# Optimization experiments

Hardware: AMD Instinct MI355X
Metric: run time of the kernel (lower is better)

The kernel has to match this reference:

```python
import jax, jax.numpy as jnp
import numpy as np


def _conv1x1(x, w, b):
    # 1x1 conv == per-pixel channel GEMM: w [Cout,Cin], x [B,C,H,W]
    return jnp.einsum('oi,bihw->bohw', w, x) + b[None, :, None, None]


def setup_inputs() -> dict:
    key = jax.random.key(0)
    ks = jax.random.split(key, 9)
    B, C, H, W = 8, 256, 128, 128
    s = 1.0 / np.sqrt(C)
    x = jax.random.normal(ks[0], (B, C, H, W), dtype=jnp.float32)
    wk = jax.random.normal(ks[1], (C, C), dtype=jnp.float32) * s
    bk = jax.random.normal(ks[2], (C,), dtype=jnp.float32) * 0.01
    wq = jax.random.normal(ks[3], (C, C), dtype=jnp.float32) * s
    bq = jax.random.normal(ks[4], (C,), dtype=jnp.float32) * 0.01
    wv = jax.random.normal(ks[5], (C, C), dtype=jnp.float32) * s
    bv = jax.random.normal(ks[6], (C,), dtype=jnp.float32) * 0.01
    wo = jax.random.normal(ks[7], (C, C), dtype=jnp.float32) * s
    bo = jax.random.normal(ks[8], (C,), dtype=jnp.float32) * 0.01
    return {'x': x, 'wk': wk, 'bk': bk, 'wq': wq, 'bq': bq,
            'wv': wv, 'bv': bv, 'wo': wo, 'bo': bo}


def reference(x, wk, bk, wq, bq, wv, bv, wo, bo):
    k = _conv1x1(x, wk, bk)   # [B,C,H,W]
    q = _conv1x1(x, wq, bq)
    v = _conv1x1(x, wv, bv)
    # transpose(key,-1,-2) @ query -> [B,C,W,W]
    scores = jnp.einsum('bchw,bchv->bcwv', k, q)
    # softmax over dim=0 (batch), as in the original module
    attn = jax.nn.softmax(scores, axis=0)
    # value @ attention_map -> [B,C,H,W]
    out = jnp.einsum('bchw,bcwv->bchv', v, attn)
    out = _conv1x1(out, wo, bo)
    return out + x
```

## Files before the change

kernel.cpp:

```cpp
#include <hip/hip_runtime.h>
#include <math.h>

#define B_ 8
#define C_ 256
#define H_ 128
#define W_ 128
#define HW_ (H_*W_)
#define PLANE ((size_t)C_*HW_)

typedef __attribute__((ext_vector_type(8))) short short8;
typedef __attribute__((ext_vector_type(4))) float f32x4;

static __device__ __forceinline__ unsigned short f2bf(float f) {
    unsigned u = __float_as_uint(f);
    u += 0x7FFF + ((u >> 16) & 1);
    return (unsigned short)(u >> 16);
}
static __device__ __forceinline__ float bf2f(unsigned short h) {
    return __uint_as_float(((unsigned)h) << 16);
}

#define SWZ(row, kbyte) ((((row) << 6) | (kbyte)) ^ (((row) & 7) << 4))

template<int NS, int MPS, bool RESID>
__global__ __launch_bounds__(256)
void conv_mfma(const float* __restrict__ X,
               const float* __restrict__ W0, const float* __restrict__ W1,
               const float* __restrict__ W2,
               const float* __restrict__ Bi0, const float* __restrict__ Bi1,
               const float* __restrict__ Bi2,
               const float* __restrict__ resid,
               float* __restrict__ Y0, float* __restrict__ Y1,
               float* __restrict__ Y2)
{
    constexpr int NROWS = NS * MPS;
    constexpr int MREP  = MPS / 16;
    constexpr int BN = 128, BK = 32;

    __shared__ unsigned short AhT[NROWS * BK], AlT[NROWS * BK];
    __shared__ unsigned short BhT[BN * BK],   BlT[BN * BK];
    __shared__ float biasLds[NROWS];

    const int b    = blockIdx.z;
    const int co0  = blockIdx.y * MPS;
    const int p0   = blockIdx.x * BN;
    const int t    = threadIdx.x;
    const int lane = t & 63;
    const int wv   = t >> 6;

    const float* Wp[3] = {W0, W1, W2};
    const float* Bp[3] = {Bi0, Bi1, Bi2};
    float*       Yp[3] = {Y0, Y1, Y2};
    const float* Xb = X + (size_t)b * PLANE;

    if (t < NROWS) {
        const int s = t / MPS, r = t % MPS;
        biasLds[t] = Bp[s][co0 + r];
    }

    f32x4 acc[NS][MREP][2];
#pragma unroll
    for (int s = 0; s < NS; ++s)
#pragma unroll
        for (int mr = 0; mr < MREP; ++mr)
#pragma unroll
            for (int nr = 0; nr < 2; ++nr)
                acc[s][mr][nr] = (f32x4){0.f, 0.f, 0.f, 0.f};

    const int kb = (lane >> 4) << 4;

    for (int k0 = 0; k0 < C_; k0 += BK) {
#pragma unroll
        for (int i = 0; i < NROWS / 32; ++i) {
            const int idx = t + (i << 8);
            const int row = idx >> 3;
            const int q4  = (idx & 7) << 2;
            const int s   = row / MPS;
            const int cl  = row % MPS;
            const float4 w4 = *(const float4*)(Wp[s] + (size_t)(co0 + cl) * C_ + (k0 + q4));
            const unsigned short h0 = f2bf(w4.x), h1 = f2bf(w4.y),
                                 h2 = f2bf(w4.z), h3 = f2bf(w4.w);
            const ushort4 hv = {h0, h1, h2, h3};
            const ushort4 lv = {f2bf(w4.x - bf2f(h0)), f2bf(w4.y - bf2f(h1)),
                                f2bf(w4.z - bf2f(h2)), f2bf(w4.w - bf2f(h3))};
            *(ushort4*)((char*)AhT + SWZ(row, q4 << 1)) = hv;
            *(ushort4*)((char*)AlT + SWZ(row, q4 << 1)) = lv;
        }
#pragma unroll
        for (int i = 0; i < 4; ++i) {
            const int ci = (i << 3) + (t & 7);
            const int p4 = (t >> 3) << 2;
            const float4 x4 = *(const float4*)(Xb + (size_t)(k0 + ci) * HW_ + (p0 + p4));
            const float xe[4] = {x4.x, x4.y, x4.z, x4.w};
#pragma unroll
            for (int e = 0; e < 4; ++e) {
                const unsigned short hh = f2bf(xe[e]);
                const unsigned short ll = f2bf(xe[e] - bf2f(hh));
                *(unsigned short*)((char*)BhT + SWZ(p4 + e, ci << 1)) = hh;
                *(unsigned short*)((char*)BlT + SWZ(p4 + e, ci << 1)) = ll;
            }
        }
        __syncthreads();

        short8 bfh[2], bfl[2];
        const int prow_base = (wv << 5) + (lane & 15);
#pragma unroll
        for (int nr = 0; nr < 2; ++nr) {
            const int prow = prow_base + (nr << 4);
            bfh[nr] = *(short8*)((char*)BhT + SWZ(prow, kb));
            bfl[nr] = *(short8*)((char*)BlT + SWZ(prow, kb));
        }
#pragma unroll
        for (int s = 0; s < NS; ++s) {
#pragma unroll
            for (int mr = 0; mr < MREP; ++mr) {
                const int arow = s * MPS + (mr << 4) + (lane & 15);
                const short8 afh = *(short8*)((char*)AhT + SWZ(arow, kb));
                const short8 afl = *(short8*)((char*)AlT + SWZ(arow, kb));
#pragma unroll
                for (int nr = 0; nr < 2; ++nr) {
                    acc[s][mr][nr] = __builtin_amdgcn_mfma_f32_16x16x32_bf16(
                        afh, bfh[nr], acc[s][mr][nr], 0, 0, 0);
                    acc[s][mr][nr] = __builtin_amdgcn_mfma_f32_16x16x32_bf16(
                        afh, bfl[nr], acc[s][mr][nr], 0, 0, 0);
                    acc[s][mr][nr] = __builtin_amdgcn_mfma_f32_16x16x32_bf16(
                        afl, bfh[nr], acc[s][mr][nr], 0, 0, 0);
                }
            }
        }
        __syncthreads();
    }

    const int r4   = (lane >> 4) << 2;
    const int pcol = p0 + (wv << 5) + (lane & 15);
#pragma unroll
    for (int s = 0; s < NS; ++s) {
        float* Y = Yp[s];
#pragma unroll
        for (int mr = 0; mr < MREP; ++mr) {
#pragma unroll
            for (int nr = 0; nr < 2; ++nr) {
                const f32x4 a = acc[s][mr][nr];
#pragma unroll
                for (int r = 0; r < 4; ++r) {
                    const int cl = (mr << 4) + r4 + r;
                    const int co = co0 + cl;
                    const size_t addr = (size_t)b * PLANE + (size_t)co * HW_
                                      + (size_t)(pcol + (nr << 4));
                    float val = a[r] + biasLds[s * MPS + cl];
                    if (RESID) val += resid[addr];
                    Y[addr] = val;
                }
            }
        }
    }
}

__global__ __launch_bounds__(256)
void scores_k(const float* __restrict__ Kt, float* __restrict__ Q )
{
    constexpr int BK = 32;
    __shared__ float Kl[BK][W_];
    __shared__ float Ql[BK][W_];

    const int bc = blockIdx.x;
    const float* Kp = Kt + (size_t)bc * HW_;
    const float* Qp = Q  + (size_t)bc * HW_;
    const int t  = threadIdx.x;
    const int tx = t & 15;
    const int ty = t >> 4;

    float acc[8][8];
#pragma unroll
    for (int i = 0; i < 8; ++i)
#pragma unroll
        for (int j = 0; j < 8; ++j) acc[i][j] = 0.f;

    for (int h0 = 0; h0 < H_; h0 += BK) {
#pragma unroll
        for (int i = 0; i < 4; ++i) {
            const int flat = (t + (i << 8)) << 2;
            const int hh = flat >> 7;
            const int nn = flat & (W_ - 1);
            *(float4*)&Kl[hh][nn] = *(const float4*)(Kp + (size_t)(h0 + hh) * W_ + nn);
            *(float4*)&Ql[hh][nn] = *(const float4*)(Qp + (size_t)(h0 + hh) * W_ + nn);
        }
        __syncthreads();
#pragma unroll 4
        for (int hh = 0; hh < BK; ++hh) {
            const float4 k0 = *(const float4*)&Kl[hh][ty << 3];
            const float4 k1 = *(const float4*)&Kl[hh][(ty << 3) + 4];
            const float4 q0 = *(const float4*)&Ql[hh][tx << 3];
            const float4 q1 = *(const float4*)&Ql[hh][(tx << 3) + 4];
            const float kr[8] = {k0.x, k0.y, k0.z, k0.w, k1.x, k1.y, k1.z, k1.w};
            const float qr[8] = {q0.x, q0.y, q0.z, q0.w, q1.x, q1.y, q1.z, q1.w};
#pragma unroll
            for (int i = 0; i < 8; ++i)
#pragma unroll
                for (int j = 0; j < 8; ++j)
                    acc[i][j] = fmaf(kr[i], qr[j], acc[i][j]);
        }
        __syncthreads();
    }

    float* Sp = Q + (size_t)bc * (size_t)W_ * W_;
#pragma unroll
    for (int i = 0; i < 8; ++i) {
        const size_t base = (size_t)((ty << 3) + i) * W_ + (tx << 3);
        float4 s0 = {acc[i][0], acc[i][1], acc[i][2], acc[i][3]};
        float4 s1 = {acc[i][4], acc[i][5], acc[i][6], acc[i][7]};
        *(float4*)(Sp + base)     = s0;
        *(float4*)(Sp + base + 4) = s1;
    }
}

__global__ __launch_bounds__(256)
void softmax_b_k(float* __restrict__ S)
{
    const size_t N = (size_t)C_ * W_ * W_;
    const size_t idx = ((size_t)blockIdx.x * 256 + threadIdx.x) << 2;
    if (idx >= N) return;

    float4 vals[B_];
#pragma unroll
    for (int b = 0; b < B_; ++b) vals[b] = *(const float4*)(S + (size_t)b * N + idx);

    float4 mx = vals[0];
#pragma unroll
    for (int b = 1; b < B_; ++b) {
        mx.x = fmaxf(mx.x, vals[b].x); mx.y = fmaxf(mx.y, vals[b].y);
        mx.z = fmaxf(mx.z, vals[b].z); mx.w = fmaxf(mx.w, vals[b].w);
    }
    float4 sum = {0.f, 0.f, 0.f, 0.f};
#pragma unroll
    for (int b = 0; b < B_; ++b) {
        vals[b].x = expf(vals[b].x - mx.x); sum.x += vals[b].x;
        vals[b].y = expf(vals[b].y - mx.y); sum.y += vals[b].y;
        vals[b].z = expf(vals[b].z - mx.z); sum.z += vals[b].z;
        vals[b].w = expf(vals[b].w - mx.w); sum.w += vals[b].w;
    }
    const float4 inv = {1.f / sum.x, 1.f / sum.y, 1.f / sum.z, 1.f / sum.w};
#pragma unroll
    for (int b = 0; b < B_; ++b) {
        float4 o = {vals[b].x * inv.x, vals[b].y * inv.y,
                    vals[b].z * inv.z, vals[b].w * inv.w};
        *(float4*)(S + (size_t)b * N + idx) = o;
    }
}

__global__ __launch_bounds__(256)
void av_k(float* __restrict__ V , const float* __restrict__ A)
{
    constexpr int BK = 32;
    __shared__ float Vl[BK][H_ + 4];
    __shared__ float Al[BK][W_];

    const int bc = blockIdx.x;
    float* Vp = V + (size_t)bc * HW_;
    const float* Ap = A + (size_t)bc * (size_t)W_ * W_;
    const int t  = threadIdx.x;
    const int tx = t & 15;
    const int ty = t >> 4;

    float acc[8][8];
#pragma unroll
    for (int i = 0; i < 8; ++i)
#pragma unroll
        for (int j = 0; j < 8; ++j) acc[i][j] = 0.f;

    for (int w0 = 0; w0 < W_; w0 += BK) {
#pragma unroll
        for (int i = 0; i < 4; ++i) {
            const int flat = (t + (i << 8)) << 2;
            const int ww = flat >> 7;
            const int nn = flat & (W_ - 1);
            *(float4*)&Al[ww][nn] = *(const float4*)(Ap + (size_t)(w0 + ww) * W_ + nn);
        }
#pragma unroll
        for (int i = 0; i < 4; ++i) {
            const int h  = (t >> 3) + (i << 5);
            const int ww = (t & 7) << 2;
            const float4 v4 = *(const float4*)(Vp + (size_t)h * W_ + (w0 + ww));
            Vl[ww + 0][h] = v4.x; Vl[ww + 1][h] = v4.y;
            Vl[ww + 2][h] = v4.z; Vl[ww + 3][h] = v4.w;
        }
        __syncthreads();
#pragma unroll 4
        for (int ww = 0; ww < BK; ++ww) {
            const float4 v0 = *(const float4*)&Vl[ww][ty << 3];
            const float4 v1 = *(const float4*)&Vl[ww][(ty << 3) + 4];
            const float4 a0 = *(const float4*)&Al[ww][tx << 3];
            const float4 a1 = *(const float4*)&Al[ww][(tx << 3) + 4];
            const float vr[8] = {v0.x, v0.y, v0.z, v0.w, v1.x, v1.y, v1.z, v1.w};
            const float ar[8] = {a0.x, a0.y, a0.z, a0.w, a1.x, a1.y, a1.z, a1.w};
#pragma unroll
            for (int i = 0; i < 8; ++i)
#pragma unroll
                for (int j = 0; j < 8; ++j)
                    acc[i][j] = fmaf(vr[i], ar[j], acc[i][j]);
        }
        __syncthreads();
    }

#pragma unroll
    for (int i = 0; i < 8; ++i) {
        const size_t base = (size_t)((ty << 3) + i) * W_ + (tx << 3);
        float4 s0 = {acc[i][0], acc[i][1], acc[i][2], acc[i][3]};
        float4 s1 = {acc[i][4], acc[i][5], acc[i][6], acc[i][7]};
        *(float4*)(Vp + base)     = s0;
        *(float4*)(Vp + base + 4) = s1;
    }
}

extern "C" void kernel_launch(void* const* d_in, const int* in_sizes, int n_in,
                              void* d_out, int out_size, void* d_ws, size_t ws_size,
                              hipStream_t stream)
{
    const float* x  = (const float*)d_in[0];
    const float* wk = (const float*)d_in[1];
    const float* bk = (const float*)d_in[2];
    const float* wq = (const float*)d_in[3];
    const float* bq = (const float*)d_in[4];
    const float* wv = (const float*)d_in[5];
    const float* bv = (const float*)d_in[6];
    const float* wo = (const float*)d_in[7];
    const float* bo = (const float*)d_in[8];
    float* out = (float*)d_out;

    const size_t NBUF = (size_t)B_ * PLANE;
    float* kbuf = (float*)d_ws;
    float* qbuf = kbuf + NBUF;
    float* vbuf = qbuf + NBUF;

    const dim3 gKQV(HW_ / 128, C_ / 32, B_);
    conv_mfma<3, 32, false><<<gKQV, 256, 0, stream>>>(
        x, wk, wq, wv, bk, bq, bv, nullptr, kbuf, qbuf, vbuf);

    scores_k<<<B_ * C_, 256, 0, stream>>>(kbuf, qbuf);
    softmax_b_k<<<4096, 256, 0, stream>>>(qbuf);
    av_k<<<B_ * C_, 256, 0, stream>>>(vbuf, qbuf);

    const dim3 gWO(HW_ / 128, C_ / 64, B_);
    conv_mfma<1, 64, true><<<gWO, 256, 0, stream>>>(
        vbuf, wo, nullptr, nullptr, bo, nullptr, nullptr, x, out, nullptr, nullptr);
}
```

Measured before the change: 912.0 us.

## Move per-channel attention GEMMs to split-bf16 MFMA with pre-swizzled softmax output

Replaces the scalar-FMA scores and attention-value kernels with MFMA bf16 kernels that split each fp32 operand into high and low bf16 parts and issue three MFMAs to approximate fp32 accuracy. The softmax kernel now writes its output directly as swizzled hi/lo bf16 tiles into the freed K buffer, so the AV kernel can copy them straight into LDS. The intent is to move the batched 128x128x128 GEMMs from vector ALUs onto matrix cores. The cost is extra conversion work, scattered scalar stores in the epilogues, and a small precision loss from the 3-term split.

```diff
diff --git a/kernel.cpp b/kernel.cpp
--- a/kernel.cpp
+++ b/kernel.cpp
@@ -157,67 +157,100 @@
 }
 
 __global__ __launch_bounds__(256)
-void scores_k(const float* __restrict__ Kt, float* __restrict__ Q )
+void scores_mfma(const float* __restrict__ Kt, float* __restrict__ Q)
 {
-    constexpr int BK = 32;
-    __shared__ float Kl[BK][W_];
-    __shared__ float Ql[BK][W_];
+    __shared__ unsigned short QTh[128 * 32], QTl[128 * 32];
+    __shared__ unsigned short KTh[128 * 32], KTl[128 * 32];
 
     const int bc = blockIdx.x;
     const float* Kp = Kt + (size_t)bc * HW_;
     const float* Qp = Q  + (size_t)bc * HW_;
-    const int t  = threadIdx.x;
-    const int tx = t & 15;
-    const int ty = t >> 4;
-
-    float acc[8][8];
-#pragma unroll
-    for (int i = 0; i < 8; ++i)
-#pragma unroll
-        for (int j = 0; j < 8; ++j) acc[i][j] = 0.f;
-
-    for (int h0 = 0; h0 < H_; h0 += BK) {
-#pragma unroll
-        for (int i = 0; i < 4; ++i) {
-            const int flat = (t + (i << 8)) << 2;
-            const int hh = flat >> 7;
-            const int nn = flat & (W_ - 1);
-            *(float4*)&Kl[hh][nn] = *(const float4*)(Kp + (size_t)(h0 + hh) * W_ + nn);
-            *(float4*)&Ql[hh][nn] = *(const float4*)(Qp + (size_t)(h0 + hh) * W_ + nn);
-        }
-        __syncthreads();
-#pragma unroll 4
-        for (int hh = 0; hh < BK; ++hh) {
-            const float4 k0 = *(const float4*)&Kl[hh][ty << 3];
-            const float4 k1 = *(const float4*)&Kl[hh][(ty << 3) + 4];
-            const float4 q0 = *(const float4*)&Ql[hh][tx << 3];
-            const float4 q1 = *(const float4*)&Ql[hh][(tx << 3) + 4];
-            const float kr[8] = {k0.x, k0.y, k0.z, k0.w, k1.x, k1.y, k1.z, k1.w};
-            const float qr[8] = {q0.x, q0.y, q0.z, q0.w, q1.x, q1.y, q1.z, q1.w};
-#pragma unroll
-            for (int i = 0; i < 8; ++i)
-#pragma unroll
-                for (int j = 0; j < 8; ++j)
-                    acc[i][j] = fmaf(kr[i], qr[j], acc[i][j]);
-        }
-        __syncthreads();
-    }
-
-    float* Sp = Q + (size_t)bc * (size_t)W_ * W_;
-#pragma unroll
-    for (int i = 0; i < 8; ++i) {
-        const size_t base = (size_t)((ty << 3) + i) * W_ + (tx << 3);
-        float4 s0 = {acc[i][0], acc[i][1], acc[i][2], acc[i][3]};
-        float4 s1 = {acc[i][4], acc[i][5], acc[i][6], acc[i][7]};
-        *(float4*)(Sp + base)     = s0;
-        *(float4*)(Sp + base + 4) = s1;
+    const int t = threadIdx.x, lane = t & 63, wv = t >> 6;
+
+    const int hhp = t & 15;
+    const int vc  = (t >> 4) << 3;
+    const int kb  = (lane >> 4) << 4;
+
+    f32x4 acc[2][8];
+#pragma unroll
+    for (int mr = 0; mr < 2; ++mr)
+#pragma unroll
+        for (int nr = 0; nr < 8; ++nr)
+            acc[mr][nr] = (f32x4){0.f, 0.f, 0.f, 0.f};
+
+    for (int h0 = 0; h0 < H_; h0 += 32) {
+        float qv[2][8], kv[2][8];
+#pragma unroll
+        for (int j = 0; j < 2; ++j) {
+            const int hh = h0 + (hhp << 1) + j;
+            const float4 q0 = *(const float4*)(Qp + (size_t)hh * W_ + vc);
+            const float4 q1 = *(const float4*)(Qp + (size_t)hh * W_ + vc + 4);
+            const float4 k0 = *(const float4*)(Kp + (size_t)hh * W_ + vc);
+            const float4 k1 = *(const float4*)(Kp + (size_t)hh * W_ + vc + 4);
+            qv[j][0]=q0.x; qv[j][1]=q0.y; qv[j][2]=q0.z; qv[j][3]=q0.w;
+            qv[j][4]=q1.x; qv[j][5]=q1.y; qv[j][6]=q1.z; qv[j][7]=q1.w;
+            kv[j][0]=k0.x; kv[j][1]=k0.y; kv[j][2]=k0.z; kv[j][3]=k0.w;
+            kv[j][4]=k1.x; kv[j][5]=k1.y; kv[j][6]=k1.z; kv[j][7]=k1.w;
+        }
+#pragma unroll
+        for (int e = 0; e < 8; ++e) {
+            const int v = vc + e;
+            const int off = SWZ(v, hhp << 2);
+            const unsigned short qh0 = f2bf(qv[0][e]), qh1 = f2bf(qv[1][e]);
+            const unsigned short kh0 = f2bf(kv[0][e]), kh1 = f2bf(kv[1][e]);
+            *(ushort2*)((char*)QTh + off) = (ushort2){qh0, qh1};
+            *(ushort2*)((char*)QTl + off) = (ushort2){f2bf(qv[0][e] - bf2f(qh0)),
+                                                      f2bf(qv[1][e] - bf2f(qh1))};
+            *(ushort2*)((char*)KTh + off) = (ushort2){kh0, kh1};
+            *(ushort2*)((char*)KTl + off) = (ushort2){f2bf(kv[0][e] - bf2f(kh0)),
+                                                      f2bf(kv[1][e] - bf2f(kh1))};
+        }
+        __syncthreads();
+
+        short8 bh[8], bl[8];
+#pragma unroll
+        for (int nr = 0; nr < 8; ++nr) {
+            const int wrow = (nr << 4) + (lane & 15);
+            bh[nr] = *(short8*)((char*)KTh + SWZ(wrow, kb));
+            bl[nr] = *(short8*)((char*)KTl + SWZ(wrow, kb));
+        }
+#pragma unroll
+        for (int mr = 0; mr < 2; ++mr) {
+            const int vrow = (wv << 5) + (mr << 4) + (lane & 15);
+            const short8 ah = *(short8*)((char*)QTh + SWZ(vrow, kb));
+            const short8 al = *(short8*)((char*)QTl + SWZ(vrow, kb));
+#pragma unroll
+            for (int nr = 0; nr < 8; ++nr) {
+                acc[mr][nr] = __builtin_amdgcn_mfma_f32_16x16x32_bf16(ah, bh[nr], acc[mr][nr], 0, 0, 0);
+                acc[mr][nr] = __builtin_amdgcn_mfma_f32_16x16x32_bf16(ah, bl[nr], acc[mr][nr], 0, 0, 0);
+                acc[mr][nr] = __builtin_amdgcn_mfma_f32_16x16x32_bf16(al, bh[nr], acc[mr][nr], 0, 0, 0);
+            }
+        }
+        __syncthreads();
+    }
+
+    float* Sp = Q + (size_t)bc * HW_;
+    const int r4 = (lane >> 4) << 2;
+#pragma unroll
+    for (int mr = 0; mr < 2; ++mr) {
+#pragma unroll
+        for (int nr = 0; nr < 8; ++nr) {
+            const f32x4 a = acc[mr][nr];
+            const int w = (nr << 4) + (lane & 15);
+#pragma unroll
+            for (int r = 0; r < 4; ++r) {
+                const int v = (wv << 5) + (mr << 4) + r4 + r;
+                Sp[(size_t)v * W_ + w] = a[r];
+            }
+        }
     }
 }
 
 __global__ __launch_bounds__(256)
-void softmax_b_k(float* __restrict__ S)
+void softmax_pack(const float* __restrict__ S,
+                  unsigned short* __restrict__ aH, unsigned short* __restrict__ aL)
 {
-    const size_t N = (size_t)C_ * W_ * W_;
+    const size_t N = (size_t)C_ * HW_;
     const size_t idx = ((size_t)blockIdx.x * 256 + threadIdx.x) << 2;
     if (idx >= N) return;
 
@@ -240,75 +273,108 @@
         vals[b].w = expf(vals[b].w - mx.w); sum.w += vals[b].w;
     }
     const float4 inv = {1.f / sum.x, 1.f / sum.y, 1.f / sum.z, 1.f / sum.w};
+
+    const int c = (int)(idx >> 14);
+    const int r = (int)(idx & 16383);
+    const int v = r >> 7, w = r & 127;
+    const size_t tile_byte = ((size_t)(c << 2) + (w >> 5)) * 8192 + SWZ(v, (w & 31) << 1);
+
 #pragma unroll
     for (int b = 0; b < B_; ++b) {
-        float4 o = {vals[b].x * inv.x, vals[b].y * inv.y,
-                    vals[b].z * inv.z, vals[b].w * inv.w};
-        *(float4*)(S + (size_t)b * N + idx) = o;
+        const float o0 = vals[b].x * inv.x, o1 = vals[b].y * inv.y,
+                    o2 = vals[b].z * inv.z, o3 = vals[b].w * inv.w;
+        const unsigned short h0 = f2bf(o0), h1 = f2bf(o1),
+                             h2 = f2bf(o2), h3 = f2bf(o3);
+        char* bh = (char*)(aH + (size_t)b * N) + tile_byte;
+        char* bl = (char*)(aL + (size_t)b * N) + tile_byte;
+        *(ushort4*)bh = (ushort4){h0, h1, h2, h3};
+        *(ushort4*)bl = (ushort4){f2bf(o0 - bf2f(h0)), f2bf(o1 - bf2f(h1)),
+                                  f2bf(o2 - bf2f(h2)), f2bf(o3 - bf2f(h3))};
     }
 }
 
 __global__ __launch_bounds__(256)
-void av_k(float* __restrict__ V , const float* __restrict__ A)
+void av_mfma(float* __restrict__ V,
+             const unsigned short* __restrict__ aH,
+             const unsigned short* __restrict__ aL)
 {
-    constexpr int BK = 32;
-    __shared__ float Vl[BK][H_ + 4];
-    __shared__ float Al[BK][W_];
+    __shared__ unsigned short Vh[128 * 32], Vl[128 * 32];
+    __shared__ unsigned short Ath[128 * 32], Atl[128 * 32];
 
     const int bc = blockIdx.x;
     float* Vp = V + (size_t)bc * HW_;
-    const float* Ap = A + (size_t)bc * (size_t)W_ * W_;
-    const int t  = threadIdx.x;
-    const int tx = t & 15;
-    const int ty = t >> 4;
-
-    float acc[8][8];
-#pragma unroll
-    for (int i = 0; i < 8; ++i)
-#pragma unroll
-        for (int j = 0; j < 8; ++j) acc[i][j] = 0.f;
-
-    for (int w0 = 0; w0 < W_; w0 += BK) {
-#pragma unroll
-        for (int i = 0; i < 4; ++i) {
-            const int flat = (t + (i << 8)) << 2;
-            const int ww = flat >> 7;
-            const int nn = flat & (W_ - 1);
-            *(float4*)&Al[ww][nn] = *(const float4*)(Ap + (size_t)(w0 + ww) * W_ + nn);
-        }
-#pragma unroll
-        for (int i = 0; i < 4; ++i) {
-            const int h  = (t >> 3) + (i << 5);
-            const int ww = (t & 7) << 2;
-            const float4 v4 = *(const float4*)(Vp + (size_t)h * W_ + (w0 + ww));
-            Vl[ww + 0][h] = v4.x; Vl[ww + 1][h] = v4.y;
-            Vl[ww + 2][h] = v4.z; Vl[ww + 3][h] = v4.w;
-        }
-        __syncthreads();
-#pragma unroll 4
-        for (int ww = 0; ww < BK; ++ww) {
-            const float4 v0 = *(const float4*)&Vl[ww][ty << 3];
-            const float4 v1 = *(const float4*)&Vl[ww][(ty << 3) + 4];
-            const float4 a0 = *(const float4*)&Al[ww][tx << 3];
-            const float4 a1 = *(const float4*)&Al[ww][(tx << 3) + 4];
-            const float vr[8] = {v0.x, v0.y, v0.z, v0.w, v1.x, v1.y, v1.z, v1.w};
-            const float ar[8] = {a0.x, a0.y, a0.z, a0.w, a1.x, a1.y, a1.z, a1.w};
-#pragma unroll
-            for (int i = 0; i < 8; ++i)
-#pragma unroll
-                for (int j = 0; j < 8; ++j)
-                    acc[i][j] = fmaf(vr[i], ar[j], acc[i][j]);
-        }
-        __syncthreads();
-    }
-
-#pragma unroll
-    for (int i = 0; i < 8; ++i) {
-        const size_t base = (size_t)((ty << 3) + i) * W_ + (tx << 3);
-        float4 s0 = {acc[i][0], acc[i][1], acc[i][2], acc[i][3]};
-        float4 s1 = {acc[i][4], acc[i][5], acc[i][6], acc[i][7]};
-        *(float4*)(Vp + base)     = s0;
-        *(float4*)(Vp + base + 4) = s1;
+    const int t = threadIdx.x, lane = t & 63, wv = t >> 6;
+    const int kb = (lane >> 4) << 4;
+
+    const int hrow = t >> 1;
+    const int wc   = (t & 1) << 4;
+
+    f32x4 acc[2][8];
+#pragma unroll
+    for (int mr = 0; mr < 2; ++mr)
+#pragma unroll
+        for (int nr = 0; nr < 8; ++nr)
+            acc[mr][nr] = (f32x4){0.f, 0.f, 0.f, 0.f};
+
+    for (int ks = 0; ks < 4; ++ks) {
+        const int w0 = ks << 5;
+#pragma unroll
+        for (int f = 0; f < 4; ++f) {
+            const int wl = wc + (f << 2);
+            const float4 v4 = *(const float4*)(Vp + (size_t)hrow * W_ + w0 + wl);
+            const unsigned short h0 = f2bf(v4.x), h1 = f2bf(v4.y),
+                                 h2 = f2bf(v4.z), h3 = f2bf(v4.w);
+            const int off = SWZ(hrow, wl << 1);
+            *(ushort4*)((char*)Vh + off) = (ushort4){h0, h1, h2, h3};
+            *(ushort4*)((char*)Vl + off) = (ushort4){f2bf(v4.x - bf2f(h0)), f2bf(v4.y - bf2f(h1)),
+                                                     f2bf(v4.z - bf2f(h2)), f2bf(v4.w - bf2f(h3))};
+        }
+        {
+            const size_t tb = ((size_t)(bc << 2) + ks) << 12;
+            const uint4* gh = (const uint4*)(aH + tb);
+            const uint4* gl = (const uint4*)(aL + tb);
+            ((uint4*)Ath)[t]       = gh[t];
+            ((uint4*)Ath)[t + 256] = gh[t + 256];
+            ((uint4*)Atl)[t]       = gl[t];
+            ((uint4*)Atl)[t + 256] = gl[t + 256];
+        }
+        __syncthreads();
+
+        short8 bh[8], bl[8];
+#pragma unroll
+        for (int nr = 0; nr < 8; ++nr) {
+            const int vrow = (nr << 4) + (lane & 15);
+            bh[nr] = *(short8*)((char*)Ath + SWZ(vrow, kb));
+            bl[nr] = *(short8*)((char*)Atl + SWZ(vrow, kb));
+        }
+#pragma unroll
+        for (int mr = 0; mr < 2; ++mr) {
+            const int hr = (wv << 5) + (mr << 4) + (lane & 15);
+            const short8 ah = *(short8*)((char*)Vh + SWZ(hr, kb));
+            const short8 al = *(short8*)((char*)Vl + SWZ(hr, kb));
+#pragma unroll
+            for (int nr = 0; nr < 8; ++nr) {
+                acc[mr][nr] = __builtin_amdgcn_mfma_f32_16x16x32_bf16(ah, bh[nr], acc[mr][nr], 0, 0, 0);
+                acc[mr][nr] = __builtin_amdgcn_mfma_f32_16x16x32_bf16(ah, bl[nr], acc[mr][nr], 0, 0, 0);
+                acc[mr][nr] = __builtin_amdgcn_mfma_f32_16x16x32_bf16(al, bh[nr], acc[mr][nr], 0, 0, 0);
+            }
+        }
+        __syncthreads();
+    }
+
+    const int r4 = (lane >> 4) << 2;
+#pragma unroll
+    for (int mr = 0; mr < 2; ++mr) {
+#pragma unroll
+        for (int nr = 0; nr < 8; ++nr) {
+            const f32x4 a = acc[mr][nr];
+            const int vcol = (nr << 4) + (lane & 15);
+#pragma unroll
+            for (int r = 0; r < 4; ++r) {
+                const int h = (wv << 5) + (mr << 4) + r4 + r;
+                Vp[(size_t)h * W_ + vcol] = a[r];
+            }
+        }
     }
 }
 
@@ -331,14 +397,16 @@
     float* kbuf = (float*)d_ws;
     float* qbuf = kbuf + NBUF;
     float* vbuf = qbuf + NBUF;
+    unsigned short* attnH = (unsigned short*)kbuf;
+    unsigned short* attnL = attnH + NBUF;
 
     const dim3 gKQV(HW_ / 128, C_ / 32, B_);
     conv_mfma<3, 32, false><<<gKQV, 256, 0, stream>>>(
         x, wk, wq, wv, bk, bq, bv, nullptr, kbuf, qbuf, vbuf);
 
-    scores_k<<<B_ * C_, 256, 0, stream>>>(kbuf, qbuf);
-    softmax_b_k<<<4096, 256, 0, stream>>>(qbuf);
-    av_k<<<B_ * C_, 256, 0, stream>>>(vbuf, qbuf);
+    scores_mfma<<<B_ * C_, 256, 0, stream>>>(kbuf, qbuf);
+    softmax_pack<<<4096, 256, 0, stream>>>(qbuf, attnH, attnL);
+    av_mfma<<<B_ * C_, 256, 0, stream>>>(vbuf, attnH, attnL);
 
     const dim3 gWO(HW_ / 128, C_ / 64, B_);
     conv_mfma<1, 64, true><<<gWO, 256, 0, stream>>>(
```

Result: faster. 870.4 us (-4.6%).
